# Optimization experiments

Hardware: AMD Instinct MI355X
Metric: run time of the kernel (lower is better)

Reference implementation:

```python
import jax, jax.numpy as jnp
import numpy as np
from jax import lax

B, NS, SL, NF = 1024, 9, 36, 7
H, DM, DH, FFN = 2, 128, 64, 2048
EPS = 1e-5


def setup_inputs():
    ks = jax.random.split(jax.random.key(0), 12)
    r = lambda i, shape, s=0.05: jax.random.normal(ks[i], shape, dtype=jnp.float32) * s
    return {
        "x": jax.random.normal(ks[0], (B, NS, SL, NF), dtype=jnp.float32),
        "W_g1": r(1, (NS, 64)), "b_g1": jnp.zeros((64,), jnp.float32),
        "W_g2": r(2, (64, DM)), "b_g2": jnp.zeros((DM,), jnp.float32),
        "conv1_w": r(3, (64, NF, 5)), "conv1_b": jnp.zeros((64,), jnp.float32),
        "conv2_w": r(4, (DM, 64, 3)), "conv2_b": jnp.zeros((DM,), jnp.float32),
        "bn_g": jnp.ones((DM,), jnp.float32), "bn_b": jnp.zeros((DM,), jnp.float32),
        "bn_m": jnp.zeros((DM,), jnp.float32), "bn_v": jnp.ones((DM,), jnp.float32),
        "in_proj_w": r(5, (2, 3 * DM, DM)), "in_proj_b": jnp.zeros((2, 3 * DM), jnp.float32),
        "out_proj_w": r(6, (2, DM, DM)), "out_proj_b": jnp.zeros((2, DM), jnp.float32),
        "ln1_g": jnp.ones((2, DM), jnp.float32), "ln1_b": jnp.zeros((2, DM), jnp.float32),
        "ln2_g": jnp.ones((2, DM), jnp.float32), "ln2_b": jnp.zeros((2, DM), jnp.float32),
        "ffn_w1": r(7, (2, FFN, DM)), "ffn_b1": jnp.zeros((2, FFN), jnp.float32),
        "ffn_w2": r(8, (2, DM, FFN)), "ffn_b2": jnp.zeros((2, DM), jnp.float32),
        "attn_w": r(9, (DM, 1)), "attn_b": jnp.zeros((1,), jnp.float32),
        "fc_w": r(10, (DM, 1)), "fc_b": jnp.zeros((1,), jnp.float32),
    }


def _ln(z, g, b):
    m = jnp.mean(z, -1, keepdims=True)
    v = jnp.mean(jnp.square(z - m), -1, keepdims=True)
    return (z - m) * lax.rsqrt(v + EPS) * g + b


def _gcn_agg(h):
    # Fully-connected 9-node graph (softmax(adj) > 0 everywhere, incl. self loops):
    # GCN norm deg=9 -> rows 0..8 become the mean of rows 0..8.
    # Remaining rows only receive the add_remaining_self_loops self loop (deg=1) -> identity.
    return h.at[:NS].set(jnp.mean(h[:NS], axis=0, keepdims=True))


def _forward(x, W_g1, b_g1, W_g2, b_g2, conv1_w, conv1_b, conv2_w, conv2_b,
             bn_g, bn_b, bn_m, bn_v, in_proj_w, in_proj_b, out_proj_w, out_proj_b,
             ln1_g, ln1_b, ln2_g, ln2_b, ffn_w1, ffn_b1, ffn_w2, ffn_b2,
             attn_w, attn_b, fc_w, fc_b):
    Bx = x.shape[0]
    # ---- GCN branch (edge weights from softmax(adj) are never used by GCNConv) ----
    xg = jnp.mean(x, axis=-1).reshape(Bx * SL, NS)                 # (B*36, 9)
    h = jax.nn.relu(_gcn_agg(xg @ W_g1) + b_g1)                    # (B*36, 64)
    h = jax.nn.relu(_gcn_agg(h @ W_g2) + b_g2)                     # (B*36, 128)
    x_gcn = h.reshape(Bx, SL, DM)
    # ---- conv branch ----
    xc = x.reshape(Bx * NS, NF, SL)
    dn = ("NCH", "OIH", "NCH")
    c = lax.conv_general_dilated(xc, conv1_w, (1,), [(2, 2)], dimension_numbers=dn) + conv1_b[:, None]
    c = lax.conv_general_dilated(c, conv2_w, (1,), [(1, 1)], dimension_numbers=dn) + conv2_b[:, None]
    c = (c - bn_m[:, None]) * lax.rsqrt(bn_v[:, None] + EPS) * bn_g[:, None] + bn_b[:, None]
    # AdaptiveAvgPool1d(36) on length-36 input is identity; eval-mode dropout is identity.
    s = c.reshape(Bx, NS, DM, SL).mean(axis=1).transpose(0, 2, 1)  # (B, 36, 128) batch-first
    # ---- post-LN transformer encoder (torch defaults, eval mode) ----
    scale = 1.0 / np.sqrt(DH).astype(np.float32)
    for i in range(2):
        qkv = s @ in_proj_w[i].T + in_proj_b[i]                    # (B, 36, 384)
        q, k, v = jnp.split(qkv, 3, axis=-1)
        q = q.reshape(Bx, SL, H, DH).transpose(0, 2, 1, 3)
        k = k.reshape(Bx, SL, H, DH).transpose(0, 2, 1, 3)
        v = v.reshape(Bx, SL, H, DH).transpose(0, 2, 1, 3)
        a = jax.nn.softmax(jnp.einsum("bhqd,bhkd->bhqk", q, k) * scale, axis=-1)
        o = jnp.einsum("bhqk,bhkd->bhqd", a, v).transpose(0, 2, 1, 3).reshape(Bx, SL, DM)
        o = o @ out_proj_w[i].T + out_proj_b[i]
        s = _ln(s + o, ln1_g[i], ln1_b[i])
        f = jax.nn.relu(s @ ffn_w1[i].T + ffn_b1[i]) @ ffn_w2[i].T + ffn_b2[i]
        s = _ln(s + f, ln2_g[i], ln2_b[i])
    # ---- fuse branches + attention pooling + head ----
    s = s + x_gcn
    aw = jax.nn.softmax(s @ attn_w + attn_b, axis=1)               # softmax over seq dim
    pooled = jnp.sum(s * aw, axis=1)                               # (B, 128)
    out = pooled @ fc_w + fc_b                                     # (B, 1)
    return jnp.where(out >= 0, out, 0.1 * out)                     # LeakyReLU(0.1)


def reference(x, W_g1, b_g1, W_g2, b_g2, conv1_w, conv1_b, conv2_w, conv2_b,
              bn_g, bn_b, bn_m, bn_v, in_proj_w, in_proj_b, out_proj_w, out_proj_b,
              ln1_g, ln1_b, ln2_g, ln2_b, ffn_w1, ffn_b1, ffn_w2, ffn_b2,
              attn_w, attn_b, fc_w, fc_b):
    return _forward(x, W_g1, b_g1, W_g2, b_g2, conv1_w, conv1_b, conv2_w, conv2_b,
                    bn_g, bn_b, bn_m, bn_v, in_proj_w, in_proj_b, out_proj_w, out_proj_b,
                    ln1_g, ln1_b, ln2_g, ln2_b, ffn_w1, ffn_b1, ffn_w2, ffn_b2,
                    attn_w, attn_b, fc_w, fc_b)
```

## Files before the change

kernel.cpp:

```cpp
#include <hip/hip_runtime.h>
#include <math.h>

#define EPSV   1e-5f

typedef __attribute__((ext_vector_type(8))) short bf16x8;
typedef __attribute__((ext_vector_type(4))) float f32x4;

__device__ __forceinline__ short f2bf(float f){
    unsigned u = __float_as_uint(f);
    u += 0x7fffu + ((u >> 16) & 1u);
    return (short)(u >> 16);
}
__device__ __forceinline__ f32x4 mfma16(bf16x8 a, bf16x8 b, f32x4 c){
    return __builtin_amdgcn_mfma_f32_16x16x32_bf16(a, b, c, 0, 0, 0);
}
__device__ __forceinline__ bf16x8 ldfrag(const short* base, int row, int kbyte, int rowBytes){
    int byte = row * rowBytes + kbyte;
    byte ^= (row & 7) << 4;
    return *(const bf16x8*)((const char*)base + byte);
}
__device__ __forceinline__ bf16x8 ldfragG(const short* base, int row, int kbyte, int rowBytes){
    return *(const bf16x8*)((const char*)base + (size_t)row * rowBytes + kbyte);
}
__device__ __forceinline__ void stswz(short* base, int row, int col, int rowBytes, short v){
    int byte = row * rowBytes + col * 2;
    byte ^= (row & 7) << 4;
    *(short*)((char*)base + byte) = v;
}

__global__ __launch_bounds__(256) void cvt_all(
    const float* __restrict__ ipw, const float* __restrict__ opw,
    const float* __restrict__ fw1, const float* __restrict__ fw2,
    short* __restrict__ dst)
{
    int i = (blockIdx.x * 256 + threadIdx.x) * 4;
    if (i >= 1179648) return;
    const float* src; int off;
    if (i < 98304)       { src = ipw; off = i; }
    else if (i < 131072) { src = opw; off = i - 98304; }
    else if (i < 655360) { src = fw1; off = i - 131072; }
    else {
        int o  = i - 655360;
        int L  = o >> 18;
        int oo = o & 262143;
        int s0 = oo & 7;
        int lg = (oo >> 3) & 3;
        int c  = (oo >> 5) & 127;
        int grp = oo >> 12;
        int n  = grp * 32 + ((s0 >> 2) << 4) + lg * 4;
        src = fw2; off = L * 262144 + c * 2048 + n;
        float4 v = *(const float4*)(src + off);
        short4 s;
        s.x = f2bf(v.x); s.y = f2bf(v.y); s.z = f2bf(v.z); s.w = f2bf(v.w);
        *(short4*)(dst + i) = s;
        return;
    }
    float4 v = *(const float4*)(src + off);
    short4 s;
    s.x = f2bf(v.x); s.y = f2bf(v.y); s.z = f2bf(v.z); s.w = f2bf(v.w);
    *(short4*)(dst + i) = s;
}

__global__ __launch_bounds__(256) void gcn_all(
    const float* __restrict__ x,
    const float* __restrict__ Wg1, const float* __restrict__ bg1,
    const float* __restrict__ Wg2, const float* __restrict__ bg2,
    float* __restrict__ xgcn)
{
    int tid = threadIdx.x;
    if (blockIdx.x == 18432) {
        __shared__ float xgm[9];
        __shared__ float h1s[64];
        if (tid < 9) {
            float s = 0.f;
            for (int r = 0; r < 9; ++r) {
                const float* xp = x + (r * 9 + tid) * 7;
                #pragma unroll
                for (int f = 0; f < 7; ++f) s += xp[f];
            }
            xgm[tid] = s * (1.f / 63.f);
        }
        __syncthreads();
        if (tid < 64) {
            float acc = bg1[tid];
            #pragma unroll
            for (int j = 0; j < 9; ++j) acc += xgm[j] * Wg1[j * 64 + tid];
            h1s[tid] = fmaxf(acc, 0.f);
        }
        __syncthreads();
        if (tid < 128) {
            float acc = bg2[tid];
            #pragma unroll 8
            for (int c = 0; c < 64; ++c) acc += h1s[c] * Wg2[c * 128 + tid];
            float v = fmaxf(acc, 0.f);
            for (int r = 0; r < 9; ++r) xgcn[r * 128 + tid] = v;
        }
        return;
    }

    __shared__ float xg[2][9];
    __shared__ float h1[2][64];
    int ri = tid >> 7;
    int tr = tid & 127;
    int row = blockIdx.x * 2 + ri;

    if (tr < 9) {
        const float* xp = x + (row * 9 + tr) * 7;
        float s = 0.f;
        #pragma unroll
        for (int f = 0; f < 7; ++f) s += xp[f];
        xg[ri][tr] = s * (1.f / 7.f);
    }
    __syncthreads();
    if (tr < 64) {
        float acc = bg1[tr];
        #pragma unroll
        for (int j = 0; j < 9; ++j) acc += xg[ri][j] * Wg1[j * 64 + tr];
        h1[ri][tr] = fmaxf(acc, 0.f);
    }
    __syncthreads();
    if (row >= 9) {
        float acc = bg2[tr];
        #pragma unroll 8
        for (int c = 0; c < 64; ++c) acc += h1[ri][c] * Wg2[c * 128 + tr];
        xgcn[row * 128 + tr] = fmaxf(acc, 0.f);
    }
}

__global__ __launch_bounds__(256) void conv_branch(
    const float* __restrict__ x,
    const float* __restrict__ w1, const float* __restrict__ cb1,
    const float* __restrict__ w2, const float* __restrict__ cb2,
    const float* __restrict__ bng, const float* __restrict__ bnb,
    const float* __restrict__ bnm, const float* __restrict__ bnv,
    float* __restrict__ sbuf)
{
    __shared__ float xm[7 * 40];
    __shared__ float w1s[64 * 35];
    __shared__ float o1[64 * 38];
    int tid = threadIdx.x;
    int b = blockIdx.x;

    for (int idx = tid; idx < 7 * 40; idx += 256) xm[idx] = 0.f;
    for (int idx = tid; idx < 64 * 38; idx += 256) o1[idx] = 0.f;
    for (int idx = tid; idx < 2240; idx += 256) w1s[idx] = w1[idx];
    __syncthreads();

    const float* xb = x + (size_t)b * 2268;
    for (int idx = tid; idx < 252; idx += 256) {
        int f = idx / 36, l = idx - f * 36;
        float s = 0.f;
        #pragma unroll
        for (int n = 0; n < 9; ++n) s += xb[n * 252 + idx];
        xm[f * 40 + l + 2] = s * (1.f / 9.f);
    }
    __syncthreads();

    {
        int o = tid & 63, lh = tid >> 6;
        int l0 = lh * 9;
        float acc[9];
        float bias = cb1[o];
        #pragma unroll
        for (int r = 0; r < 9; ++r) acc[r] = bias;
        #pragma unroll
        for (int i = 0; i < 7; ++i) {
            #pragma unroll
            for (int k = 0; k < 5; ++k) {
                float w = w1s[o * 35 + i * 5 + k];
                const float* xrow = &xm[i * 40 + l0 + k];
                #pragma unroll
                for (int r = 0; r < 9; ++r) acc[r] += w * xrow[r];
            }
        }
        #pragma unroll
        for (int r = 0; r < 9; ++r) o1[o * 38 + l0 + r + 1] = acc[r];
    }
    __syncthreads();

    {
        int c = tid & 127, lh = tid >> 7;
        int l0 = lh * 18;
        float acc[18];
        #pragma unroll
        for (int r = 0; r < 18; ++r) acc[r] = 0.f;
        const float* w2c = w2 + c * 192;
        for (int i = 0; i < 64; ++i) {
            float wa = w2c[i * 3 + 0], wb = w2c[i * 3 + 1], wc = w2c[i * 3 + 2];
            const float* orow = &o1[i * 38 + l0];
            #pragma unroll
            for (int r = 0; r < 18; ++r)
                acc[r] += wa * orow[r] + wb * orow[r + 1] + wc * orow[r + 2];
        }
        float scale = bng[c] * rsqrtf(bnv[c] + EPSV);
        float shift = bnb[c] - bnm[c] * scale;
        float bias  = cb2[c];
        float* sb = sbuf + ((size_t)b * 36 + l0) * 128 + c;
        #pragma unroll
        for (int r = 0; r < 18; ++r)
            sb[r * 128] = (acc[r] + bias) * scale + shift;
    }
}

__global__ __launch_bounds__(256, 2) void attn_mfma(
    float* __restrict__ sbuf,
    const short* __restrict__ ipwb, const float* __restrict__ ipb,
    const short* __restrict__ opwb, const float* __restrict__ opb,
    const float* __restrict__ l1g, const float* __restrict__ l1b)
{
    __shared__ short Sb[48 * 128] __attribute__((aligned(16)));
    __shared__ char  U[38912]     __attribute__((aligned(16)));
    __shared__ float scf[36 * 40];
    short* Qb = (short*)U;
    short* Kb = (short*)(U + 6144);
    short* Vt = (short*)(U + 12288);
    short* Pb = (short*)(U + 20480);
    short* Hb = (short*)(U + 26624);

    const int tid  = threadIdx.x;
    const int wid  = tid >> 6;
    const int lane = tid & 63;
    const int lr   = lane & 15;
    const int lg   = lane >> 4;
    const int kbse = lg * 16;

    float* sg = sbuf + (size_t)blockIdx.x * 4608;
    const f32x4 fzero = {0.f, 0.f, 0.f, 0.f};

    for (int idx = tid; idx < 4608; idx += 256) {
        int r = idx >> 7, c = idx & 127;
        stswz(Sb, r, c, 256, f2bf(sg[idx]));
    }
    for (int idx = tid; idx < 1024; idx += 256)
        stswz(Vt, idx >> 4, 48 + (idx & 15), 128, 0);
    __syncthreads();

    for (int h = 0; h < 2; ++h) {
        {
            f32x4 acc[3][3];
            #pragma unroll
            for (int a = 0; a < 3; ++a)
                #pragma unroll
                for (int m = 0; m < 3; ++m) acc[a][m] = fzero;
            const int wrow0 = h * 64 + wid * 16 + lr;
            #pragma unroll
            for (int ks = 0; ks < 4; ++ks) {
                bf16x8 a0 = ldfrag(Sb,      lr, ks * 64 + kbse, 256);
                bf16x8 a1 = ldfrag(Sb, 16 + lr, ks * 64 + kbse, 256);
                bf16x8 a2 = ldfrag(Sb, 32 + lr, ks * 64 + kbse, 256);
                #pragma unroll
                for (int mat = 0; mat < 3; ++mat) {
                    bf16x8 bf = ldfragG(ipwb, mat * 128 + wrow0, ks * 64 + kbse, 256);
                    acc[mat][0] = mfma16(a0, bf, acc[mat][0]);
                    acc[mat][1] = mfma16(a1, bf, acc[mat][1]);
                    acc[mat][2] = mfma16(a2, bf, acc[mat][2]);
                }
            }
            int col = wid * 16 + lr;
            #pragma unroll
            for (int mat = 0; mat < 3; ++mat) {
                float bias = ipb[mat * 128 + h * 64 + col];
                #pragma unroll
                for (int mt = 0; mt < 3; ++mt) {
                    f32x4 c4 = acc[mat][mt];
                    if (mat == 0) {
                        #pragma unroll
                        for (int j = 0; j < 4; ++j)
                            stswz(Qb, mt * 16 + lg * 4 + j, col, 128, f2bf(c4[j] + bias));
                    } else if (mat == 1) {
                        #pragma unroll
                        for (int j = 0; j < 4; ++j)
                            stswz(Kb, mt * 16 + lg * 4 + j, col, 128, f2bf(c4[j] + bias));
                    } else {
                        int rbase = mt * 16 + lg * 4;
                        short4 s4;
                        s4.x = f2bf(rbase + 0 < 36 ? c4[0] + bias : 0.f);
                        s4.y = f2bf(rbase + 1 < 36 ? c4[1] + bias : 0.f);
                        s4.z = f2bf(rbase + 2 < 36 ? c4[2] + bias : 0.f);
                        s4.w = f2bf(rbase + 3 < 36 ? c4[3] + bias : 0.f);
                        int byte = col * 128 + rbase * 2;
                        byte ^= (col & 7) << 4;
                        *(short4*)((char*)Vt + byte) = s4;
                    }
                }
            }
        }
        __syncthreads();

        for (int t = wid; t < 9; t += 4) {
            int mt = t / 3, nt = t - mt * 3;
            f32x4 acc = fzero;
            #pragma unroll
            for (int ks = 0; ks < 2; ++ks) {
                bf16x8 a = ldfrag(Qb, mt * 16 + lr, ks * 64 + kbse, 128);
                bf16x8 b = ldfrag(Kb, nt * 16 + lr, ks * 64 + kbse, 128);
                acc = mfma16(a, b, acc);
            }
            int col = nt * 16 + lr;
            if (col < 36) {
                #pragma unroll
                for (int j = 0; j < 4; ++j) {
                    int r = mt * 16 + lg * 4 + j;
                    if (r < 36) scf[r * 40 + col] = acc[j] * 0.125f;
                }
            }
        }
        __syncthreads();

        {
            int g = tid >> 2, e = tid & 3;
            if (g < 36) {
                float v[9];
                float mx = -1e30f;
                #pragma unroll
                for (int i = 0; i < 9; ++i) { v[i] = scf[g * 40 + e * 9 + i]; mx = fmaxf(mx, v[i]); }
                mx = fmaxf(mx, __shfl_xor(mx, 1));
                mx = fmaxf(mx, __shfl_xor(mx, 2));
                float ssum = 0.f;
                #pragma unroll
                for (int i = 0; i < 9; ++i) { v[i] = __expf(v[i] - mx); ssum += v[i]; }
                ssum += __shfl_xor(ssum, 1);
                ssum += __shfl_xor(ssum, 2);
                float inv = 1.f / ssum;
                #pragma unroll
                for (int i = 0; i < 9; ++i)
                    stswz(Pb, g, e * 9 + i, 128, f2bf(v[i] * inv));
                #pragma unroll
                for (int i = 0; i < 7; ++i)
                    stswz(Pb, g, 36 + e * 7 + i, 128, 0);
            }
        }
        __syncthreads();

        {
            f32x4 oacc[3] = {fzero, fzero, fzero};
            #pragma unroll
            for (int ks = 0; ks < 2; ++ks) {
                bf16x8 b = ldfrag(Vt, wid * 16 + lr, ks * 64 + kbse, 128);
                #pragma unroll
                for (int mt = 0; mt < 3; ++mt) {
                    bf16x8 a = ldfrag(Pb, mt * 16 + lr, ks * 64 + kbse, 128);
                    oacc[mt] = mfma16(a, b, oacc[mt]);
                }
            }
            int col = h * 64 + wid * 16 + lr;
            #pragma unroll
            for (int mt = 0; mt < 3; ++mt)
                #pragma unroll
                for (int j = 0; j < 4; ++j)
                    stswz(Hb, mt * 16 + lg * 4 + j, col, 256, f2bf(oacc[mt][j]));
        }
        __syncthreads();
    }

    float z[3][2][4];
    {
        f32x4 pacc[3][2];
        #pragma unroll
        for (int m = 0; m < 3; ++m) { pacc[m][0] = fzero; pacc[m][1] = fzero; }
        #pragma unroll
        for (int ks = 0; ks < 4; ++ks) {
            bf16x8 a0 = ldfrag(Hb,      lr, ks * 64 + kbse, 256);
            bf16x8 a1 = ldfrag(Hb, 16 + lr, ks * 64 + kbse, 256);
            bf16x8 a2 = ldfrag(Hb, 32 + lr, ks * 64 + kbse, 256);
            #pragma unroll
            for (int t = 0; t < 2; ++t) {
                bf16x8 b = ldfragG(opwb, (wid * 2 + t) * 16 + lr, ks * 64 + kbse, 256);
                pacc[0][t] = mfma16(a0, b, pacc[0][t]);
                pacc[1][t] = mfma16(a1, b, pacc[1][t]);
                pacc[2][t] = mfma16(a2, b, pacc[2][t]);
            }
        }
        #pragma unroll
        for (int t = 0; t < 2; ++t) {
            int col = (wid * 2 + t) * 16 + lr;
            float bias = opb[col];
            #pragma unroll
            for (int mt = 0; mt < 3; ++mt)
                #pragma unroll
                for (int j = 0; j < 4; ++j) {
                    int r = mt * 16 + lg * 4 + j;
                    z[mt][t][j] = (r < 36) ? pacc[mt][t][j] + bias + sg[r * 128 + col] : 0.f;
                }
        }
    }
    {
        float* part = scf;
        #pragma unroll
        for (int mt = 0; mt < 3; ++mt)
            #pragma unroll
            for (int j = 0; j < 4; ++j) {
                int r = mt * 16 + lg * 4 + j;
                float s  = z[mt][0][j] + z[mt][1][j];
                float ss = z[mt][0][j] * z[mt][0][j] + z[mt][1][j] * z[mt][1][j];
                s  += __shfl_xor(s, 1);  s  += __shfl_xor(s, 2);
                s  += __shfl_xor(s, 4);  s  += __shfl_xor(s, 8);
                ss += __shfl_xor(ss, 1); ss += __shfl_xor(ss, 2);
                ss += __shfl_xor(ss, 4); ss += __shfl_xor(ss, 8);
                if (lr == 0 && r < 36) { part[r * 8 + wid] = s; part[r * 8 + 4 + wid] = ss; }
            }
    }
    __syncthreads();
    {
        const float* part = scf;
        #pragma unroll
        for (int mt = 0; mt < 3; ++mt)
            #pragma unroll
            for (int j = 0; j < 4; ++j) {
                int r = mt * 16 + lg * 4 + j;
                if (r < 36) {
                    float s  = part[r * 8 + 0] + part[r * 8 + 1] + part[r * 8 + 2] + part[r * 8 + 3];
                    float ss = part[r * 8 + 4] + part[r * 8 + 5] + part[r * 8 + 6] + part[r * 8 + 7];
                    float mean = s * (1.f / 128.f);
                    float rstd = rsqrtf(ss * (1.f / 128.f) - mean * mean + EPSV);
                    #pragma unroll
                    for (int t = 0; t < 2; ++t) {
                        int col = (wid * 2 + t) * 16 + lr;
                        float v = (z[mt][t][j] - mean) * rstd * l1g[col] + l1b[col];
                        sg[r * 128 + col] = v;
                    }
                }
            }
    }
}

__global__ __launch_bounds__(256, 4) void ffn_v5(
    float* __restrict__ sres,
    const short* __restrict__ fw1b, const float* __restrict__ fb1,
    const short* __restrict__ fw2p, const float* __restrict__ fb2,
    const float* __restrict__ l2g, const float* __restrict__ l2b)
{
    __shared__ short Wbuf[2][8192] __attribute__((aligned(16)));

    const int tid  = threadIdx.x;
    const int wid  = tid >> 6;
    const int lane = tid & 63;
    const int lr   = lane & 15;
    const int lg   = lane >> 4;
    const size_t row0 = (size_t)blockIdx.x * 64 + wid * 16;
    const f32x4 fzero = {0.f, 0.f, 0.f, 0.f};

    bf16x8 sfrag[4];
    {
        const float* sp = sres + (row0 + lr) * 128;
        #pragma unroll
        for (int ks = 0; ks < 4; ++ks) {
            float4 lo = *(const float4*)(sp + ks * 32 + lg * 8);
            float4 hi = *(const float4*)(sp + ks * 32 + lg * 8 + 4);
            bf16x8 f;
            f[0] = f2bf(lo.x); f[1] = f2bf(lo.y); f[2] = f2bf(lo.z); f[3] = f2bf(lo.w);
            f[4] = f2bf(hi.x); f[5] = f2bf(hi.y); f[6] = f2bf(hi.z); f[7] = f2bf(hi.w);
            sfrag[ks] = f;
        }
    }

    f32x4 facc[8];
    #pragma unroll
    for (int ct = 0; ct < 8; ++ct) facc[ct] = fzero;

    bf16x8 g1[2], g2[2];
    #pragma unroll
    for (int i = 0; i < 2; ++i) {
        int fid = tid + 256 * i;
        g1[i] = *(const bf16x8*)((const char*)fw1b + fid * 16);
        g2[i] = *(const bf16x8*)((const char*)fw2p + fid * 16);
    }
    #pragma unroll
    for (int i = 0; i < 2; ++i) {
        int fid = tid + 256 * i;
        int swz = (fid * 16) ^ (((fid >> 4) & 7) << 4);
        *(bf16x8*)((char*)&Wbuf[0][0] + swz)         = g1[i];
        *(bf16x8*)((char*)&Wbuf[0][4096] + fid * 16) = g2[i];
    }

#define FFN_CHUNK(Q, CUR, NXT)                                                    \
    {                                                                             \
        const int q = (Q);                                                        \
        if (q < 63) {                                                             \
            const char* b1p = (const char*)fw1b + (q + 1) * 8192;                 \
            const char* b2p = (const char*)fw2p + (q + 1) * 8192;                 \
            _Pragma("unroll")                                                     \
            for (int i = 0; i < 2; ++i) {                                         \
                int fid = tid + 256 * i;                                          \
                g1[i] = *(const bf16x8*)(b1p + fid * 16);                         \
                g2[i] = *(const bf16x8*)(b2p + fid * 16);                         \
            }                                                                     \
        }                                                                         \
        __syncthreads();                 \
        const short* W1l = &Wbuf[CUR][0];                                         \
        const short* W2l = &Wbuf[CUR][4096];                                      \
                   \
        f32x4 hacc[2];                                                            \
        hacc[0] = fzero; hacc[1] = fzero;                                         \
        _Pragma("unroll")                                                         \
        for (int ks = 0; ks < 4; ++ks) {                                          \
            bf16x8 a0 = ldfrag(W1l,      lr, ks * 64 + lg * 16, 256);             \
            bf16x8 a1 = ldfrag(W1l, 16 + lr, ks * 64 + lg * 16, 256);             \
            hacc[0] = mfma16(a0, sfrag[ks], hacc[0]);                             \
            hacc[1] = mfma16(a1, sfrag[ks], hacc[1]);                             \
        }                                                                         \
                 \
        float4 bA = *(const float4*)(fb1 + q * 32 + lg * 4);                      \
        float4 bB = *(const float4*)(fb1 + q * 32 + 16 + lg * 4);                 \
        bf16x8 hf;                                                                \
        hf[0] = f2bf(fmaxf(hacc[0][0] + bA.x, 0.f));                              \
        hf[1] = f2bf(fmaxf(hacc[0][1] + bA.y, 0.f));                              \
        hf[2] = f2bf(fmaxf(hacc[0][2] + bA.z, 0.f));                              \
        hf[3] = f2bf(fmaxf(hacc[0][3] + bA.w, 0.f));                              \
        hf[4] = f2bf(fmaxf(hacc[1][0] + bB.x, 0.f));                              \
        hf[5] = f2bf(fmaxf(hacc[1][1] + bB.y, 0.f));                              \
        hf[6] = f2bf(fmaxf(hacc[1][2] + bB.z, 0.f));                              \
        hf[7] = f2bf(fmaxf(hacc[1][3] + bB.w, 0.f));                              \
         \
        _Pragma("unroll")                                                         \
        for (int ct = 0; ct < 8; ++ct) {                                          \
            bf16x8 b2 = *(const bf16x8*)(W2l + ((ct * 16 + lr) * 4 + lg) * 8);    \
            facc[ct] = mfma16(hf, b2, facc[ct]);                                  \
        }                                                                         \
        if (q < 63) {                                                             \
            char* d1 = (char*)&Wbuf[NXT][0];                                      \
            char* d2 = (char*)&Wbuf[NXT][4096];                                   \
            _Pragma("unroll")                                                     \
            for (int i = 0; i < 2; ++i) {                                         \
                int fid = tid + 256 * i;                                          \
                int swz = (fid * 16) ^ (((fid >> 4) & 7) << 4);                   \
                *(bf16x8*)(d1 + swz)        = g1[i];                              \
                *(bf16x8*)(d2 + fid * 16)   = g2[i];                              \
            }                                                                     \
        }                                                                         \
    }

    #pragma unroll 1
    for (int qq = 0; qq < 32; ++qq) {
        FFN_CHUNK(2 * qq,     0, 1)
        FFN_CHUNK(2 * qq + 1, 1, 0)
    }
#undef FFN_CHUNK

    float zv[8][4];
    #pragma unroll
    for (int ct = 0; ct < 8; ++ct) {
        int c = ct * 16 + lr;
        float b2v = fb2[c];
        #pragma unroll
        for (int j = 0; j < 4; ++j)
            zv[ct][j] = facc[ct][j] + b2v + sres[(row0 + lg * 4 + j) * 128 + c];
    }
    #pragma unroll
    for (int j = 0; j < 4; ++j) {
        float s = 0.f, sq = 0.f;
        #pragma unroll
        for (int ct = 0; ct < 8; ++ct) { s += zv[ct][j]; sq += zv[ct][j] * zv[ct][j]; }
        s  += __shfl_xor(s, 1);  s  += __shfl_xor(s, 2);
        s  += __shfl_xor(s, 4);  s  += __shfl_xor(s, 8);
        sq += __shfl_xor(sq, 1); sq += __shfl_xor(sq, 2);
        sq += __shfl_xor(sq, 4); sq += __shfl_xor(sq, 8);
        float mean = s * (1.f / 128.f);
        float rstd = rsqrtf(sq * (1.f / 128.f) - mean * mean + EPSV);
        float* og = sres + (row0 + lg * 4 + j) * 128;
        #pragma unroll
        for (int ct = 0; ct < 8; ++ct) {
            int c = ct * 16 + lr;
            og[c] = (zv[ct][j] - mean) * rstd * l2g[c] + l2b[c];
        }
    }
}

__global__ __launch_bounds__(128) void pool_head(
    const float* __restrict__ sbuf, const float* __restrict__ xgcn,
    const float* __restrict__ aww, const float* __restrict__ awb,
    const float* __restrict__ fcw, const float* __restrict__ fcb,
    float* __restrict__ out)
{
    __shared__ float sl[36][128];
    __shared__ float zz[36];
    __shared__ float p[128];
    int tid = threadIdx.x;
    int b = blockIdx.x;
    const float* sg = sbuf + (size_t)b * 4608;
    const float* gg = xgcn + (size_t)b * 4608;
    for (int idx = tid; idx < 4608; idx += 128)
        sl[0][idx] = sg[idx] + gg[idx];
    __syncthreads();
    if (tid < 36) {
        float acc = awb[0];
        #pragma unroll
        for (int j = 0; j < 128; j += 4) {
            float4 s4 = *(const float4*)&sl[tid][j];
            float4 w4 = *(const float4*)(aww + j);
            acc += s4.x * w4.x + s4.y * w4.y + s4.z * w4.z + s4.w * w4.w;
        }
        zz[tid] = acc;
    }
    __syncthreads();
    if (tid == 0) {
        float m = -1e30f;
        for (int k = 0; k < 36; ++k) m = fmaxf(m, zz[k]);
        float ssum = 0.f;
        for (int k = 0; k < 36; ++k) ssum += __expf(zz[k] - m);
        float inv = 1.f / ssum;
        for (int k = 0; k < 36; ++k) zz[k] = __expf(zz[k] - m) * inv;
    }
    __syncthreads();
    {
        float acc = 0.f;
        for (int l = 0; l < 36; ++l) acc += sl[l][tid] * zz[l];
        p[tid] = acc;
    }
    __syncthreads();
    if (tid == 0) {
        float acc = fcb[0];
        for (int dd = 0; dd < 128; ++dd) acc += p[dd] * fcw[dd];
        out[b] = acc >= 0.f ? acc : 0.1f * acc;
    }
}

extern "C" void kernel_launch(void* const* d_in, const int* in_sizes, int n_in,
                              void* d_out, int out_size, void* d_ws, size_t ws_size,
                              hipStream_t stream)
{
    const float* x   = (const float*)d_in[0];
    const float* Wg1 = (const float*)d_in[1];
    const float* bg1 = (const float*)d_in[2];
    const float* Wg2 = (const float*)d_in[3];
    const float* bg2 = (const float*)d_in[4];
    const float* c1w = (const float*)d_in[5];
    const float* c1b = (const float*)d_in[6];
    const float* c2w = (const float*)d_in[7];
    const float* c2b = (const float*)d_in[8];
    const float* bng = (const float*)d_in[9];
    const float* bnb = (const float*)d_in[10];
    const float* bnm = (const float*)d_in[11];
    const float* bnv = (const float*)d_in[12];
    const float* ipw = (const float*)d_in[13];
    const float* ipb = (const float*)d_in[14];
    const float* opw = (const float*)d_in[15];
    const float* opb = (const float*)d_in[16];
    const float* l1g = (const float*)d_in[17];
    const float* l1b = (const float*)d_in[18];
    const float* l2g = (const float*)d_in[19];
    const float* l2b = (const float*)d_in[20];
    const float* fw1 = (const float*)d_in[21];
    const float* fb1 = (const float*)d_in[22];
    const float* fw2 = (const float*)d_in[23];
    const float* fb2 = (const float*)d_in[24];
    const float* aww = (const float*)d_in[25];
    const float* awb = (const float*)d_in[26];
    const float* fcw = (const float*)d_in[27];
    const float* fcb = (const float*)d_in[28];
    float* out = (float*)d_out;

    float* sbuf = (float*)d_ws;
    float* xgcn = sbuf + (size_t)1024 * 36 * 128;
    short* wb   = (short*)(xgcn + (size_t)1024 * 36 * 128);
    short* ipwb = wb;
    short* opwb = wb + 98304;
    short* fw1b = wb + 131072;
    short* fw2p = wb + 655360;

    cvt_all<<<1152, 256, 0, stream>>>(ipw, opw, fw1, fw2, wb);
    gcn_all<<<18433, 256, 0, stream>>>(x, Wg1, bg1, Wg2, bg2, xgcn);
    conv_branch<<<1024, 256, 0, stream>>>(x, c1w, c1b, c2w, c2b,
                                          bng, bnb, bnm, bnv, sbuf);
    for (int i = 0; i < 2; ++i) {
        attn_mfma<<<1024, 256, 0, stream>>>(sbuf,
            ipwb + (size_t)i * 49152, ipb + (size_t)i * 384,
            opwb + (size_t)i * 16384, opb + (size_t)i * 128,
            l1g + (size_t)i * 128, l1b + (size_t)i * 128);
        ffn_v5<<<576, 256, 0, stream>>>(sbuf,
            fw1b + (size_t)i * 262144, fb1 + (size_t)i * 2048,
            fw2p + (size_t)i * 262144, fb2 + (size_t)i * 128,
            l2g + (size_t)i * 128, l2b + (size_t)i * 128);
    }
    pool_head<<<1024, 128, 0, stream>>>(sbuf, xgcn, aww, awb, fcw, fcb, out);
}
```

Baseline: 337.0 us.

## Shrink attention LDS for 3 blocks/CU and swizzle FFN W2 LDS tile

The attention kernel packs its shared buffers into one tighter arena sized for 36 rows instead of 48. It raises launch bounds from 2 to 3 blocks per CU, and Q/K/H stores are masked to the 36 valid rows so padding rows are not written. In the FFN kernel, the W2 staging tile gets an XOR swizzle on both store and load to avoid LDS bank conflicts. The higher occupancy target may limit registers per thread and cause spills, and the reads of padding rows now depend on data that is never written.

```diff
diff --git a/kernel.cpp b/kernel.cpp
--- a/kernel.cpp
+++ b/kernel.cpp
@@ -202,20 +202,20 @@
     }
 }
 
-__global__ __launch_bounds__(256, 2) void attn_mfma(
+__global__ __launch_bounds__(256, 3) void attn_mfma(
     float* __restrict__ sbuf,
     const short* __restrict__ ipwb, const float* __restrict__ ipb,
     const short* __restrict__ opwb, const float* __restrict__ opb,
     const float* __restrict__ l1g, const float* __restrict__ l1b)
 {
-    __shared__ short Sb[48 * 128] __attribute__((aligned(16)));
-    __shared__ char  U[38912]     __attribute__((aligned(16)));
-    __shared__ float scf[36 * 40];
-    short* Qb = (short*)U;
-    short* Kb = (short*)(U + 6144);
-    short* Vt = (short*)(U + 12288);
-    short* Pb = (short*)(U + 20480);
-    short* Hb = (short*)(U + 26624);
+    __shared__ char AR[46208] __attribute__((aligned(16)));
+    short* Sb = (short*)(AR);
+    short* Qb = (short*)(AR + 9216);
+    short* Kb = (short*)(AR + 13824);
+    short* Vt = (short*)(AR + 18432);
+    short* Pb = (short*)(AR + 26624);
+    short* Hb = (short*)(AR + 31232);
+    float* scf = (float*)(AR + 40448);
 
     const int tid  = threadIdx.x;
     const int wid  = tid >> 6;
@@ -265,12 +265,16 @@
                     f32x4 c4 = acc[mat][mt];
                     if (mat == 0) {
                         #pragma unroll
-                        for (int j = 0; j < 4; ++j)
-                            stswz(Qb, mt * 16 + lg * 4 + j, col, 128, f2bf(c4[j] + bias));
+                        for (int j = 0; j < 4; ++j) {
+                            int r = mt * 16 + lg * 4 + j;
+                            if (r < 36) stswz(Qb, r, col, 128, f2bf(c4[j] + bias));
+                        }
                     } else if (mat == 1) {
                         #pragma unroll
-                        for (int j = 0; j < 4; ++j)
-                            stswz(Kb, mt * 16 + lg * 4 + j, col, 128, f2bf(c4[j] + bias));
+                        for (int j = 0; j < 4; ++j) {
+                            int r = mt * 16 + lg * 4 + j;
+                            if (r < 36) stswz(Kb, r, col, 128, f2bf(c4[j] + bias));
+                        }
                     } else {
                         int rbase = mt * 16 + lg * 4;
                         short4 s4;
@@ -347,8 +351,10 @@
             #pragma unroll
             for (int mt = 0; mt < 3; ++mt)
                 #pragma unroll
-                for (int j = 0; j < 4; ++j)
-                    stswz(Hb, mt * 16 + lg * 4 + j, col, 256, f2bf(oacc[mt][j]));
+                for (int j = 0; j < 4; ++j) {
+                    int r = mt * 16 + lg * 4 + j;
+                    if (r < 36) stswz(Hb, r, col, 256, f2bf(oacc[mt][j]));
+                }
         }
         __syncthreads();
     }
@@ -468,9 +474,11 @@
     #pragma unroll
     for (int i = 0; i < 2; ++i) {
         int fid = tid + 256 * i;
-        int swz = (fid * 16) ^ (((fid >> 4) & 7) << 4);
-        *(bf16x8*)((char*)&Wbuf[0][0] + swz)         = g1[i];
-        *(bf16x8*)((char*)&Wbuf[0][4096] + fid * 16) = g2[i];
+        int b1 = fid * 16;
+        int s1 = b1 ^ (((b1 >> 8) & 7) << 4);
+        int s2 = b1 ^ (((b1 >> 7) & 3) << 4);
+        *(bf16x8*)((char*)&Wbuf[0][0] + s1)    = g1[i];
+        *(bf16x8*)((char*)&Wbuf[0][4096] + s2) = g2[i];
     }
 
 #define FFN_CHUNK(Q, CUR, NXT)                                                    \
@@ -511,11 +519,13 @@
         hf[5] = f2bf(fmaxf(hacc[1][1] + bB.y, 0.f));                              \
         hf[6] = f2bf(fmaxf(hacc[1][2] + bB.z, 0.f));                              \
         hf[7] = f2bf(fmaxf(hacc[1][3] + bB.w, 0.f));                              \
-         \
+               \
         _Pragma("unroll")                                                         \
         for (int ct = 0; ct < 8; ++ct) {                                          \
-            bf16x8 b2 = *(const bf16x8*)(W2l + ((ct * 16 + lr) * 4 + lg) * 8);    \
-            facc[ct] = mfma16(hf, b2, facc[ct]);                                  \
+            int wb2 = ((ct * 16 + lr) * 4 + lg) * 16;                             \
+            wb2 ^= ((lr >> 1) & 3) << 4;                                          \
+            bf16x8 b2f = *(const bf16x8*)((const char*)W2l + wb2);                \
+            facc[ct] = mfma16(hf, b2f, facc[ct]);                                 \
         }                                                                         \
         if (q < 63) {                                                             \
             char* d1 = (char*)&Wbuf[NXT][0];                                      \
@@ -523,9 +533,11 @@
             _Pragma("unroll")                                                     \
             for (int i = 0; i < 2; ++i) {                                         \
                 int fid = tid + 256 * i;                                          \
-                int swz = (fid * 16) ^ (((fid >> 4) & 7) << 4);                   \
-                *(bf16x8*)(d1 + swz)        = g1[i];                              \
-                *(bf16x8*)(d2 + fid * 16)   = g2[i];                              \
+                int b1 = fid * 16;                                                \
+                int s1 = b1 ^ (((b1 >> 8) & 7) << 4);                             \
+                int s2 = b1 ^ (((b1 >> 7) & 3) << 4);                             \
+                *(bf16x8*)(d1 + s1) = g1[i];                                      \
+                *(bf16x8*)(d2 + s2) = g2[i];                                      \
             }                                                                     \
         }                                                                         \
     }
```

Result: no change. 335.0 us (-0.6%).
